# Kernel tuning notes

Measured on AMD Instinct MI355X. Metric: run time of the kernel, lower is better.

Reference implementation:

```python
import jax, jax.numpy as jnp
import numpy as np

K, OUT, IN = 4, 4096, 4096
B, S = 2, 2048

def setup_inputs() -> dict:
    key = jax.random.key(0)
    k1, k2, k3 = jax.random.split(key, 3)
    x = jax.random.normal(k1, (B, S, IN), dtype=jnp.float32)
    alphas = jax.random.normal(k2, (K,), dtype=jnp.float32)
    # binary bases in {-1, +1}, stored as int8 like the torch buffer
    bases = (jax.random.randint(k3, (K, OUT, IN), 0, 2) * 2 - 1).astype(jnp.int8)
    return {"x": x, "alphas": alphas, "bases": bases}

def reference(x, alphas, bases):
    # W_q = sum_i alphas[i] * bases[i]  -> [out, in]
    W_q = jnp.einsum('k,koi->oi', alphas, bases.astype(x.dtype))
    # y = x @ W_q.T  -> [B, S, out]
    return jnp.einsum('bsi,oi->bso', x, W_q)
```

## Files before the change

### kernel.cpp

```cpp
#include <hip/hip_runtime.h>
#include <hip/hip_bf16.h>
#include <stdint.h>

#define DIM_M 4096
#define DIM_N 4096
#define DIM_K 4096
#define BASE_STRIDE (DIM_N * DIM_K)

typedef __bf16 bf16x8 __attribute__((ext_vector_type(8)));
typedef float floatx4 __attribute__((ext_vector_type(4)));
typedef unsigned short ushort8 __attribute__((ext_vector_type(8)));

__device__ __forceinline__ unsigned short f2bf(float f) {
    uint32_t u = __float_as_uint(f);
    uint32_t r = (u + 0x7FFFu + ((u >> 16) & 1u)) >> 16;
    return (unsigned short)r;
}

__global__ __launch_bounds__(256) void prep_kernel(
        const int* __restrict__ bases, const float* __restrict__ alphas,
        const float* __restrict__ x,
        unsigned short* __restrict__ Wb, unsigned short* __restrict__ Xb) {
    const int bid = blockIdx.x;
    if (bid < 8192) {
        const long e = ((long)bid * 256 + threadIdx.x) * 8;
        const float a0 = alphas[0], a1 = alphas[1], a2 = alphas[2], a3 = alphas[3];
        const int4 p0 = *(const int4*)(bases + e);
        const int4 p1 = *(const int4*)(bases + e + 4);
        const int4 q0 = *(const int4*)(bases + BASE_STRIDE + e);
        const int4 q1 = *(const int4*)(bases + BASE_STRIDE + e + 4);
        const int4 r0 = *(const int4*)(bases + 2L * BASE_STRIDE + e);
        const int4 r1 = *(const int4*)(bases + 2L * BASE_STRIDE + e + 4);
        const int4 s0 = *(const int4*)(bases + 3L * BASE_STRIDE + e);
        const int4 s1 = *(const int4*)(bases + 3L * BASE_STRIDE + e + 4);
        ushort8 o;
        o[0] = f2bf(a0 * p0.x + a1 * q0.x + a2 * r0.x + a3 * s0.x);
        o[1] = f2bf(a0 * p0.y + a1 * q0.y + a2 * r0.y + a3 * s0.y);
        o[2] = f2bf(a0 * p0.z + a1 * q0.z + a2 * r0.z + a3 * s0.z);
        o[3] = f2bf(a0 * p0.w + a1 * q0.w + a2 * r0.w + a3 * s0.w);
        o[4] = f2bf(a0 * p1.x + a1 * q1.x + a2 * r1.x + a3 * s1.x);
        o[5] = f2bf(a0 * p1.y + a1 * q1.y + a2 * r1.y + a3 * s1.y);
        o[6] = f2bf(a0 * p1.z + a1 * q1.z + a2 * r1.z + a3 * s1.z);
        o[7] = f2bf(a0 * p1.w + a1 * q1.w + a2 * r1.w + a3 * s1.w);
        *(ushort8*)(Wb + e) = o;
    } else {
        const long e = ((long)(bid - 8192) * 256 + threadIdx.x) * 8;
        const float4 v0 = *(const float4*)(x + e);
        const float4 v1 = *(const float4*)(x + e + 4);
        ushort8 o;
        o[0] = f2bf(v0.x); o[1] = f2bf(v0.y); o[2] = f2bf(v0.z); o[3] = f2bf(v0.w);
        o[4] = f2bf(v1.x); o[5] = f2bf(v1.y); o[6] = f2bf(v1.z); o[7] = f2bf(v1.w);
        *(ushort8*)(Xb + e) = o;
    }
}

__global__ __launch_bounds__(256) void gemm_bt_kernel(
        const unsigned short* __restrict__ A, const unsigned short* __restrict__ Bt,
        float* __restrict__ C) {
    __shared__ unsigned short sA[2 * 128 * 32];
    __shared__ unsigned short sB[2 * 128 * 32];

    const int t = threadIdx.x;
    const int wave = t >> 6, lane = t & 63;
    const int wm = (wave >> 1) * 64;
    const int wn = (wave & 1) * 64;
    const int quad = lane >> 4, l16 = lane & 15;

    const int mBase = blockIdx.y * 128;
    const int nBase = blockIdx.x * 128;

    const int srow = t >> 2;
    const int qc = (t & 3) ^ ((t >> 3) & 3);
    const unsigned short* gA0 = A + (size_t)(mBase + srow) * DIM_K + qc * 8;
    const unsigned short* gA1 = gA0 + (size_t)64 * DIM_K;
    const unsigned short* gB0 = Bt + (size_t)(nBase + srow) * DIM_K + qc * 8;
    const unsigned short* gB1 = gB0 + (size_t)64 * DIM_K;

    const int swz = quad ^ ((l16 >> 1) & 3);
    const int aoff0 = (wm + l16) * 32 + swz * 8;
    const int boff0 = (wn + l16) * 32 + swz * 8;

    floatx4 acc[4][4] = {};

    ushort8 rA0 = *(const ushort8*)gA0;
    ushort8 rA1 = *(const ushort8*)gA1;
    ushort8 rB0 = *(const ushort8*)gB0;
    ushort8 rB1 = *(const ushort8*)gB1;
    gA0 += 32; gA1 += 32; gB0 += 32; gB1 += 32;
    *(ushort8*)(sA + t * 8) = rA0;
    *(ushort8*)(sA + 2048 + t * 8) = rA1;
    *(ushort8*)(sB + t * 8) = rB0;
    *(ushort8*)(sB + 2048 + t * 8) = rB1;
    __syncthreads();

    int p = 0;
    for (int kt = 0; kt < DIM_K; kt += 32) {
        const bool more = (kt + 32) < DIM_K;
        if (more) {
            rA0 = *(const ushort8*)gA0;
            rA1 = *(const ushort8*)gA1;
            rB0 = *(const ushort8*)gB0;
            rB1 = *(const ushort8*)gB1;
            gA0 += 32; gA1 += 32; gB0 += 32; gB1 += 32;
        }

        const unsigned short* bufA = sA + p * 4096;
        const unsigned short* bufB = sB + p * 4096;
        bf16x8 a[4], b[4];
#pragma unroll
        for (int i = 0; i < 4; i++)
            a[i] = *(const bf16x8*)(bufA + aoff0 + i * 16 * 32);
#pragma unroll
        for (int j = 0; j < 4; j++)
            b[j] = *(const bf16x8*)(bufB + boff0 + j * 16 * 32);

#pragma unroll
        for (int i = 0; i < 4; i++)
#pragma unroll
            for (int j = 0; j < 4; j++)
                acc[i][j] = __builtin_amdgcn_mfma_f32_16x16x32_bf16(
                    a[i], b[j], acc[i][j], 0, 0, 0);

        if (more) {
            unsigned short* wA = sA + (p ^ 1) * 4096;
            unsigned short* wB = sB + (p ^ 1) * 4096;
            *(ushort8*)(wA + t * 8) = rA0;
            *(ushort8*)(wA + 2048 + t * 8) = rA1;
            *(ushort8*)(wB + t * 8) = rB0;
            *(ushort8*)(wB + 2048 + t * 8) = rB1;
        }
        __syncthreads();
        p ^= 1;
    }

#pragma unroll
    for (int i = 0; i < 4; i++) {
#pragma unroll
        for (int j = 0; j < 4; j++) {
#pragma unroll
            for (int r = 0; r < 4; r++) {
                const int row = mBase + wm + i * 16 + quad * 4 + r;
                const int col = nBase + wn + j * 16 + l16;
                C[(size_t)row * DIM_N + col] = acc[i][j][r];
            }
        }
    }
}

__global__ __launch_bounds__(256) void naive_kernel(
        const float* __restrict__ x, const float* __restrict__ alphas,
        const int* __restrict__ bases, float* __restrict__ out) {
    const long o = (long)blockIdx.x * 256 + threadIdx.x;
    const int m = (int)(o >> 12), n = (int)(o & 4095);
    const float a0 = alphas[0], a1 = alphas[1], a2 = alphas[2], a3 = alphas[3];
    const float* xr = x + (long)m * DIM_K;
    const int* b0 = bases + (long)n * DIM_K;
    const int* b1 = b0 + BASE_STRIDE;
    const int* b2 = b1 + BASE_STRIDE;
    const int* b3 = b2 + BASE_STRIDE;
    float acc = 0.f;
    for (int i = 0; i < DIM_K; i++) {
        float w = a0 * b0[i] + a1 * b1[i] + a2 * b2[i] + a3 * b3[i];
        acc += xr[i] * w;
    }
    out[o] = acc;
}

extern "C" void kernel_launch(void* const* d_in, const int* in_sizes, int n_in,
                              void* d_out, int out_size, void* d_ws, size_t ws_size,
                              hipStream_t stream) {
    const float* x      = (const float*)d_in[0];
    const float* alphas = (const float*)d_in[1];
    const int*   bases  = (const int*)d_in[2];
    float* out = (float*)d_out;

    const size_t need = (size_t)2 * DIM_N * DIM_K + (size_t)2 * DIM_M * DIM_K;
    if (ws_size >= need) {
        unsigned short* Wb = (unsigned short*)d_ws;
        unsigned short* Xb = (unsigned short*)d_ws + (size_t)DIM_N * DIM_K;
        prep_kernel<<<16384, 256, 0, stream>>>(bases, alphas, x, Wb, Xb);
        gemm_bt_kernel<<<dim3(DIM_N / 128, DIM_M / 128), 256, 0, stream>>>(Xb, Wb, out);
    } else {
        naive_kernel<<<(DIM_M * DIM_N) / 256, 256, 0, stream>>>(x, alphas, bases, out);
    }
}
```

Baseline: 599.4 us.

## Switch GEMM to 32x32x16 MFMA with XCD-aware block remapping

```diff
diff --git a/kernel.cpp b/kernel.cpp
--- a/kernel.cpp
+++ b/kernel.cpp
@@ -8,7 +8,7 @@
 #define BASE_STRIDE (DIM_N * DIM_K)
 
 typedef __bf16 bf16x8 __attribute__((ext_vector_type(8)));
-typedef float floatx4 __attribute__((ext_vector_type(4)));
+typedef float floatx16 __attribute__((ext_vector_type(16)));
 typedef unsigned short ushort8 __attribute__((ext_vector_type(8)));
 
 __device__ __forceinline__ unsigned short f2bf(float f) {
@@ -54,7 +54,7 @@
     }
 }
 
-__global__ __launch_bounds__(256) void gemm_bt_kernel(
+__global__ __launch_bounds__(256, 4) void gemm_bt_kernel(
         const unsigned short* __restrict__ A, const unsigned short* __restrict__ Bt,
         float* __restrict__ C) {
     __shared__ unsigned short sA[2 * 128 * 32];
@@ -64,10 +64,13 @@
     const int wave = t >> 6, lane = t & 63;
     const int wm = (wave >> 1) * 64;
     const int wn = (wave & 1) * 64;
-    const int quad = lane >> 4, l16 = lane & 15;
+    const int l31 = lane & 31, g = lane >> 5;
 
-    const int mBase = blockIdx.y * 128;
-    const int nBase = blockIdx.x * 128;
+    const int f = blockIdx.x;
+    const int tm = (f >> 3) & 31;
+    const int tn = (f & 7) * 4 + (f >> 8);
+    const int mBase = tm * 128;
+    const int nBase = tn * 128;
 
     const int srow = t >> 2;
     const int qc = (t & 3) ^ ((t >> 3) & 3);
@@ -76,11 +79,13 @@
     const unsigned short* gB0 = Bt + (size_t)(nBase + srow) * DIM_K + qc * 8;
     const unsigned short* gB1 = gB0 + (size_t)64 * DIM_K;
 
-    const int swz = quad ^ ((l16 >> 1) & 3);
-    const int aoff0 = (wm + l16) * 32 + swz * 8;
-    const int boff0 = (wn + l16) * 32 + swz * 8;
+    const int s = (l31 >> 1) & 3;
+    const int c0 = ((0 + g) ^ s) * 8;
+    const int c1 = ((2 + g) ^ s) * 8;
+    const int arow = (wm + l31) * 32;
+    const int brow = (wn + l31) * 32;
 
-    floatx4 acc[4][4] = {};
+    floatx16 acc[2][2] = {};
 
     ushort8 rA0 = *(const ushort8*)gA0;
     ushort8 rA1 = *(const ushort8*)gA1;
@@ -106,20 +111,26 @@
 
         const unsigned short* bufA = sA + p * 4096;
         const unsigned short* bufB = sB + p * 4096;
-        bf16x8 a[4], b[4];
+        bf16x8 a[2][2], b[2][2];
 #pragma unroll
-        for (int i = 0; i < 4; i++)
-            a[i] = *(const bf16x8*)(bufA + aoff0 + i * 16 * 32);
+        for (int i = 0; i < 2; i++) {
+            a[i][0] = *(const bf16x8*)(bufA + arow + i * 32 * 32 + c0);
+            a[i][1] = *(const bf16x8*)(bufA + arow + i * 32 * 32 + c1);
+        }
 #pragma unroll
-        for (int j = 0; j < 4; j++)
-            b[j] = *(const bf16x8*)(bufB + boff0 + j * 16 * 32);
+        for (int j = 0; j < 2; j++) {
+            b[j][0] = *(const bf16x8*)(bufB + brow + j * 32 * 32 + c0);
+            b[j][1] = *(const bf16x8*)(bufB + brow + j * 32 * 32 + c1);
+        }
 
 #pragma unroll
-        for (int i = 0; i < 4; i++)
+        for (int h = 0; h < 2; h++)
 #pragma unroll
-            for (int j = 0; j < 4; j++)
-                acc[i][j] = __builtin_amdgcn_mfma_f32_16x16x32_bf16(
-                    a[i], b[j], acc[i][j], 0, 0, 0);
+            for (int i = 0; i < 2; i++)
+#pragma unroll
+                for (int j = 0; j < 2; j++)
+                    acc[i][j] = __builtin_amdgcn_mfma_f32_32x32x16_bf16(
+                        a[i][h], b[j][h], acc[i][j], 0, 0, 0);
 
         if (more) {
             unsigned short* wA = sA + (p ^ 1) * 4096;
@@ -134,13 +145,13 @@
     }
 
 #pragma unroll
-    for (int i = 0; i < 4; i++) {
+    for (int i = 0; i < 2; i++) {
 #pragma unroll
-        for (int j = 0; j < 4; j++) {
+        for (int j = 0; j < 2; j++) {
 #pragma unroll
-            for (int r = 0; r < 4; r++) {
-                const int row = mBase + wm + i * 16 + quad * 4 + r;
-                const int col = nBase + wn + j * 16 + l16;
+            for (int r = 0; r < 16; r++) {
+                const int row = mBase + wm + i * 32 + (r & 3) + 8 * (r >> 2) + 4 * g;
+                const int col = nBase + wn + j * 32 + l31;
                 C[(size_t)row * DIM_N + col] = acc[i][j][r];
             }
         }
@@ -179,7 +190,7 @@
         unsigned short* Wb = (unsigned short*)d_ws;
         unsigned short* Xb = (unsigned short*)d_ws + (size_t)DIM_N * DIM_K;
         prep_kernel<<<16384, 256, 0, stream>>>(bases, alphas, x, Wb, Xb);
-        gemm_bt_kernel<<<dim3(DIM_N / 128, DIM_M / 128), 256, 0, stream>>>(Xb, Wb, out);
+        gemm_bt_kernel<<<1024, 256, 0, stream>>>(Xb, Wb, out);
     } else {
         naive_kernel<<<(DIM_M * DIM_N) / 256, 256, 0, stream>>>(x, alphas, bases, out);
     }
```

Result: no change. 594.7 us (-0.8%).
